# Kernel tuning notes

Hardware: AMD Instinct MI355X
Metric: run time of the kernel (lower is better)

## Reference

```python
import jax, jax.numpy as jnp
import numpy as np

B, T1, H, P, V = 4096, 65, 64, 50, 32
D = H + P  # input_size = 114


def setup_inputs() -> dict:
    key = jax.random.key(0)
    ks = jax.random.split(key, 20)
    s = 1.0 / np.sqrt(D)
    sh = 1.0 / np.sqrt(H)
    inp = {
        "phonetic_input": jax.random.normal(ks[0], (B, P), dtype=jnp.float32),
        "char_seq": jax.random.randint(ks[1], (B, T1), 0, V, dtype=jnp.int64),
        "emb": jax.random.normal(ks[2], (V, H), dtype=jnp.float32).at[0].set(0.0),  # padding_idx=0
        "W_rx": jax.random.uniform(ks[3], (D, H), jnp.float32, -s, s),
        "b_rx": jax.random.uniform(ks[4], (H,), jnp.float32, -s, s),
        "W_rh": jax.random.uniform(ks[5], (H, H), jnp.float32, -sh, sh),
        "b_rh": jax.random.uniform(ks[6], (H,), jnp.float32, -sh, sh),
        "W_zx": jax.random.uniform(ks[7], (D, H), jnp.float32, -s, s),
        "b_zx": jax.random.uniform(ks[8], (H,), jnp.float32, -s, s),
        "W_zh": jax.random.uniform(ks[9], (H, H), jnp.float32, -sh, sh),
        "b_zh": jax.random.uniform(ks[10], (H,), jnp.float32, -sh, sh),
        "W_hx": jax.random.uniform(ks[11], (D, H), jnp.float32, -s, s),
        "b_hx": jax.random.uniform(ks[12], (H,), jnp.float32, -s, s),
        "W_hh": jax.random.uniform(ks[13], (H, H), jnp.float32, -sh, sh),
        "b_hh": jax.random.uniform(ks[14], (H,), jnp.float32, -sh, sh),
        "W_proj": jax.random.uniform(ks[15], (H, V), jnp.float32, -sh, sh),
        "b_proj": jax.random.uniform(ks[16], (V,), jnp.float32, -sh, sh),
    }
    return inp


def reference(phonetic_input, char_seq, emb, W_rx, b_rx, W_rh, b_rh, W_zx, b_zx,
              W_zh, b_zh, W_hx, b_hx, W_hh, b_hh, W_proj, b_proj):
    input_seq = char_seq[:, :-1]          # [B, T]
    target_seq = char_seq[:, 1:]          # [B, T]
    Bsz, T = input_seq.shape

    char_emb = emb[input_seq]                                   # [B, T, H]
    phon = jnp.broadcast_to(phonetic_input[:, None, :], (Bsz, T, P))
    x = jnp.concatenate([char_emb, phon], axis=2)               # [B, T, D]

    # Hoist input-side projections into batched GEMMs, [T, B, H] for scan
    xr = jnp.einsum('btd,dh->tbh', x, W_rx) + b_rx
    xz = jnp.einsum('btd,dh->tbh', x, W_zx) + b_zx
    xh = jnp.einsum('btd,dh->tbh', x, W_hx) + b_hx

    h0 = jnp.zeros((Bsz, H), dtype=x.dtype)

    def step(h, inputs):
        xr_t, xz_t, xh_t = inputs
        r = jax.nn.sigmoid(xr_t + h @ W_rh + b_rh)
        z = jax.nn.sigmoid(xz_t + h @ W_zh + b_zh)
        c = jnp.tanh(xh_t + (r * h) @ W_hh + b_hh)
        h_new = (1.0 - z) * h + z * c
        return h_new, h_new

    _, hs = jax.lax.scan(step, h0, (xr, xz, xh))                # [T, B, H]
    logits = jnp.einsum('tbh,hv->btv', hs, W_proj) + b_proj     # [B, T, V]

    # cross_entropy with ignore_index=0 (mean over non-ignored)
    targets = target_seq.reshape(-1)
    logp = jax.nn.log_softmax(logits.reshape(-1, V), axis=-1)
    nll = -jnp.take_along_axis(logp, targets[:, None], axis=-1)[:, 0]
    mask = (targets != 0).astype(logits.dtype)
    loss = jnp.sum(nll * mask) / jnp.maximum(jnp.sum(mask), 1.0)
    return logits, loss
```

## Files before the change

### kernel.cpp

```cpp
#include <hip/hip_runtime.h>
#include <stdint.h>

#define Bsz 4096
#define Tn  64
#define T1n 65
#define Hn  64
#define Pn  50
#define Vn  32

typedef __attribute__((ext_vector_type(8))) short short8;
typedef __attribute__((ext_vector_type(4))) unsigned short bf16x4;
typedef __attribute__((ext_vector_type(4))) float floatx4;

__device__ __forceinline__ float bf2f(unsigned short u) {
  union { unsigned int i; float f; } x; x.i = ((unsigned int)u) << 16; return x.f;
}
__device__ __forceinline__ unsigned short f2bf(float f) {
  union { float f; unsigned int i; } x; x.f = f;
  return (unsigned short)((x.i + 0x7FFFu + ((x.i >> 16) & 1u)) >> 16);
}
__device__ __forceinline__ float fast_sigmoid(float x) {
  return __builtin_amdgcn_rcpf(1.f + __expf(-x));
}
__device__ __forceinline__ float fast_tanh(float x) {
  return 1.f - 2.f * __builtin_amdgcn_rcpf(1.f + __expf(2.f * x));
}
__device__ __forceinline__ void bar_lgkm() {
  asm volatile("s_waitcnt lgkmcnt(0)\n\ts_barrier" ::: "memory");
}

__device__ __forceinline__ short8 load_bfrag(const float* __restrict__ W, int ncols, int col, int kbase) {
  short8 f;
#pragma unroll
  for (int j = 0; j < 8; ++j) f[j] = (short)f2bf(W[(long)(kbase + j) * ncols + col]);
  return f;
}

__launch_bounds__(512)
__global__ void gru_kernel(const float* __restrict__ phon,
                           const int* __restrict__ cs,
                           const float* __restrict__ emb,
                           const float* __restrict__ Wrx, const float* __restrict__ brx,
                           const float* __restrict__ Wrh, const float* __restrict__ brh,
                           const float* __restrict__ Wzx, const float* __restrict__ bzx,
                           const float* __restrict__ Wzh, const float* __restrict__ bzh,
                           const float* __restrict__ Whx, const float* __restrict__ bhx,
                           const float* __restrict__ Whh, const float* __restrict__ bhh,
                           const float* __restrict__ Wpj, const float* __restrict__ bpj_g,
                           float* __restrict__ ws,
                           float* __restrict__ outp) {
  __shared__ __align__(16) unsigned short tbl_s[32 * 66 * 4];
  __shared__ __align__(16) unsigned short hist_s[2 * 1152];
  __shared__ __align__(16) unsigned short rh_s[1152];
  __shared__ float sum_s[32];
  __shared__ float tl_s[16];
  __shared__ unsigned int code4_s[(T1n + 1) * 4];
  __shared__ int det_s[1];

  const int tid = threadIdx.x;
  const int b0 = blockIdx.x * 16;
  const int W8 = tid >> 6, lane = tid & 63, q = lane >> 4, c16 = lane & 15;
  const bool isScan = (W8 < 4);
  const int jcol = (W8 & 3) * 16 + c16;
  const floatx4 zf = {0.f, 0.f, 0.f, 0.f};

  if (tid == 0) det_s[0] = 0;
  __syncthreads();
  if (tid < 128 && cs[2 * tid + 1] != 0) atomicOr(&det_s[0], 1);
  __syncthreads();
  const bool is64 = (det_s[0] == 0);

  for (int i = tid; i < 1152; i += 512) hist_s[1152 + i] = 0;
  for (int i = tid; i < T1n * 4; i += 512) {
    int t = i >> 2, qq = i & 3;
    unsigned int pk = 0;
#pragma unroll
    for (int r = 0; r < 4; ++r) {
      long idx = (long)(b0 + qq * 4 + r) * T1n + t;
      int c = is64 ? cs[2 * idx] : cs[idx];
      pk |= ((unsigned int)(c & 255)) << (8 * r);
    }
    code4_s[i] = pk;
  }

  for (int g = 0; g < 3; ++g) {
    const float* Wg = (g == 0) ? Wrx : (g == 1) ? Wzx : Whx;
    const float* bx = (g == 0) ? brx : (g == 1) ? bzx : bhx;
    const float* bh = (g == 0) ? brh : (g == 1) ? bzh : bhh;
    float acc[4] = {0.f, 0.f, 0.f, 0.f};
    float bias = bx[lane] + bh[lane];
    for (int d = 0; d < Hn; ++d) {
      float wv = Wg[(long)d * Hn + lane];
#pragma unroll
      for (int k = 0; k < 4; ++k)
        acc[k] += emb[(long)(W8 + 8 * k) * Hn + d] * wv;
    }
#pragma unroll
    for (int k = 0; k < 4; ++k) {
      int v = W8 + 8 * k;
      tbl_s[(v * 66 + lane) * 4 + g] = f2bf(acc[k] + bias);
    }
  }

  float ph_r[4] = {0.f, 0.f, 0.f, 0.f};
  float ph_z[4] = {0.f, 0.f, 0.f, 0.f};
  float ph_h[4] = {0.f, 0.f, 0.f, 0.f};
  if (isScan) {
    for (int p = 0; p < Pn; ++p) {
      float wr = Wrx[(long)(Hn + p) * Hn + jcol];
      float wz = Wzx[(long)(Hn + p) * Hn + jcol];
      float wh = Whx[(long)(Hn + p) * Hn + jcol];
#pragma unroll
      for (int r = 0; r < 4; ++r) {
        float xv = phon[(long)(b0 + q * 4 + r) * Pn + p];
        ph_r[r] += xv * wr; ph_z[r] += xv * wz; ph_h[r] += xv * wh;
      }
    }
  }

  short8 zs = {0,0,0,0,0,0,0,0};
  short8 Br0 = zs, Br1 = zs, Bz0 = zs, Bz1 = zs, Bh0 = zs, Bh1 = zs;
  short8 Bp0 = zs, Bp1 = zs;
  float bpj = 0.f;
  const int vt = W8 - 4;
  if (isScan) {
    Br0 = load_bfrag(Wrh, Hn, jcol, q * 8);
    Br1 = load_bfrag(Wrh, Hn, jcol, 32 + q * 8);
    Bz0 = load_bfrag(Wzh, Hn, jcol, q * 8);
    Bz1 = load_bfrag(Wzh, Hn, jcol, 32 + q * 8);
    Bh0 = load_bfrag(Whh, Hn, jcol, q * 8);
    Bh1 = load_bfrag(Whh, Hn, jcol, 32 + q * 8);
  } else if (W8 < 6) {
    Bp0 = load_bfrag(Wpj, Vn, vt * 16 + c16, q * 8);
    Bp1 = load_bfrag(Wpj, Vn, vt * 16 + c16, 32 + q * 8);
    bpj = bpj_g[vt * 16 + c16];
  }

  float h[4] = {0.f, 0.f, 0.f, 0.f};
  float z4[4] = {0.f, 0.f, 0.f, 0.f};
  float nll = 0.f, cnt = 0.f;
  bf16x4 tv[4];
  float eA[4], lgA[4];
  bool tm[4] = {false, false, false, false};

  if (isScan) {
    unsigned int pk0 = code4_s[q];
#pragma unroll
    for (int reg = 0; reg < 4; ++reg) {
      int cr = (pk0 >> (8 * reg)) & 255;
      tv[reg] = *(const bf16x4*)&tbl_s[(cr * 66 + jcol) * 4];
    }
  }

  __syncthreads();

  for (int t = 0; t < Tn + 2; ++t) {
    if (isScan) {
      if (t < Tn) {
        const unsigned short* hp = &hist_s[((t + 1) & 1) * 1152];
        short8 a0 = *(const short8*)&hp[c16 * 72 + q * 8];
        short8 a1 = *(const short8*)&hp[c16 * 72 + 32 + q * 8];
        floatx4 accr = __builtin_amdgcn_mfma_f32_16x16x32_bf16(a0, Br0, zf, 0, 0, 0);
        floatx4 accz = __builtin_amdgcn_mfma_f32_16x16x32_bf16(a0, Bz0, zf, 0, 0, 0);
        accr = __builtin_amdgcn_mfma_f32_16x16x32_bf16(a1, Br1, accr, 0, 0, 0);
        accz = __builtin_amdgcn_mfma_f32_16x16x32_bf16(a1, Bz1, accz, 0, 0, 0);
#pragma unroll
        for (int reg = 0; reg < 4; ++reg) {
          float xr = bf2f(tv[reg][0]) + ph_r[reg] + accr[reg];
          float xz = bf2f(tv[reg][1]) + ph_z[reg] + accz[reg];
          z4[reg] = fast_sigmoid(xz);
          rh_s[(q * 4 + reg) * 72 + jcol] = f2bf(fast_sigmoid(xr) * h[reg]);
        }
      }
    } else if (W8 < 6) {
      if (t >= 1 && t <= Tn) {
        const unsigned short* hp = &hist_s[((t + 1) & 1) * 1152];
        short8 a0 = *(const short8*)&hp[c16 * 72 + q * 8];
        short8 a1 = *(const short8*)&hp[c16 * 72 + 32 + q * 8];
        floatx4 l = __builtin_amdgcn_mfma_f32_16x16x32_bf16(a0, Bp0, zf, 0, 0, 0);
        l = __builtin_amdgcn_mfma_f32_16x16x32_bf16(a1, Bp1, l, 0, 0, 0);
        const int p = t - 1;
        unsigned int pkP = code4_s[t * 4 + q];
#pragma unroll
        for (int reg = 0; reg < 4; ++reg) {
          float lg = l[reg] + bpj;
          lgA[reg] = lg;
          eA[reg] = __expf(lg);
          long ad = ((long)(b0 + q * 4 + reg) * Tn + p) * Vn + vt * 16 + c16;
          outp[ad] = lg;
          int targ = (pkP >> (8 * reg)) & 255;
          tm[reg] = (targ != 0) && (targ == vt * 16 + c16);
        }
      }
    } else if (W8 == 6) {
      if (t >= 2 && lane < 16) {
        unsigned int pk6 = code4_s[(t - 1) * 4 + (lane >> 2)];
        int targ = (pk6 >> (8 * (lane & 3))) & 255;
        if (targ != 0) {
          float s = sum_s[lane] + sum_s[16 + lane];
          nll += __logf(s) - tl_s[lane];
          cnt += 1.f;
        }
      }
    }
    bar_lgkm();

    if (isScan) {
      if (t < Tn) {
        short8 p0 = *(const short8*)&rh_s[c16 * 72 + q * 8];
        short8 p1 = *(const short8*)&rh_s[c16 * 72 + 32 + q * 8];
        floatx4 acc = __builtin_amdgcn_mfma_f32_16x16x32_bf16(p0, Bh0, zf, 0, 0, 0);
        acc = __builtin_amdgcn_mfma_f32_16x16x32_bf16(p1, Bh1, acc, 0, 0, 0);
        unsigned short* hw = &hist_s[(t & 1) * 1152];
#pragma unroll
        for (int reg = 0; reg < 4; ++reg) {
          float xh = bf2f(tv[reg][2]) + ph_h[reg] + acc[reg];
          float c = fast_tanh(xh);
          float hn = fmaf(z4[reg], c - h[reg], h[reg]);
          h[reg] = hn;
          hw[(q * 4 + reg) * 72 + jcol] = f2bf(hn);
        }
        unsigned int pkN = code4_s[(t + 1) * 4 + q];
#pragma unroll
        for (int reg = 0; reg < 4; ++reg) {
          int crN = (pkN >> (8 * reg)) & 255;
          tv[reg] = *(const bf16x4*)&tbl_s[(crN * 66 + jcol) * 4];
        }
      }
    } else if (W8 < 6) {
      if (t >= 1 && t <= Tn) {
#pragma unroll
        for (int reg = 0; reg < 4; ++reg) {
          float s = eA[reg];
          s += __shfl_xor(s, 1); s += __shfl_xor(s, 2);
          s += __shfl_xor(s, 4); s += __shfl_xor(s, 8);
          if (c16 == 0) sum_s[vt * 16 + q * 4 + reg] = s;
          if (tm[reg])  tl_s[q * 4 + reg] = lgA[reg];
        }
      }
    }
    bar_lgkm();
  }

  if (W8 == 6) {
#pragma unroll
    for (int off = 8; off >= 1; off >>= 1) {
      nll += __shfl_xor(nll, off);
      cnt += __shfl_xor(cnt, off);
    }
    if (lane == 0) {
      ws[2 * blockIdx.x] = nll;
      ws[2 * blockIdx.x + 1] = cnt;
    }
  }
}

__global__ void loss_kernel(const float* __restrict__ ws, float* __restrict__ outp) {
  int lane = threadIdx.x;
  float n = 0.f, c = 0.f;
  for (int i = lane; i < Bsz / 16; i += 64) { n += ws[2 * i]; c += ws[2 * i + 1]; }
#pragma unroll
  for (int off = 32; off >= 1; off >>= 1) {
    n += __shfl_xor(n, off);
    c += __shfl_xor(c, off);
  }
  if (lane == 0) outp[(size_t)Bsz * Tn * Vn] = n / fmaxf(c, 1.f);
}

extern "C" void kernel_launch(void* const* d_in, const int* in_sizes, int n_in,
                              void* d_out, int out_size, void* d_ws, size_t ws_size,
                              hipStream_t stream) {
  const float* phon = (const float*)d_in[0];
  const int*   cs   = (const int*)d_in[1];
  const float* emb  = (const float*)d_in[2];
  const float* Wrx  = (const float*)d_in[3];
  const float* brx  = (const float*)d_in[4];
  const float* Wrh  = (const float*)d_in[5];
  const float* brh  = (const float*)d_in[6];
  const float* Wzx  = (const float*)d_in[7];
  const float* bzx  = (const float*)d_in[8];
  const float* Wzh  = (const float*)d_in[9];
  const float* bzh  = (const float*)d_in[10];
  const float* Whx  = (const float*)d_in[11];
  const float* bhx  = (const float*)d_in[12];
  const float* Whh  = (const float*)d_in[13];
  const float* bhh  = (const float*)d_in[14];
  const float* Wpj  = (const float*)d_in[15];
  const float* bpj  = (const float*)d_in[16];
  float* ws = (float*)d_ws;

  hipLaunchKernelGGL(gru_kernel, dim3(Bsz / 16), dim3(512), 0, stream,
                     phon, cs, emb, Wrx, brx, Wrh, brh, Wzx, bzx, Wzh, bzh,
                     Whx, bhx, Whh, bhh, Wpj, bpj, ws, (float*)d_out);
  hipLaunchKernelGGL(loss_kernel, dim3(1), dim3(64), 0, stream, ws, (float*)d_out);
}
```

Before: 190.1 us.

## Transpose GRU MFMA operands so hidden state packs per-lane and logits store vectorized

```diff
diff --git a/kernel.cpp b/kernel.cpp
--- a/kernel.cpp
+++ b/kernel.cpp
@@ -18,6 +18,9 @@
 __device__ __forceinline__ unsigned short f2bf(float f) {
   union { float f; unsigned int i; } x; x.f = f;
   return (unsigned short)((x.i + 0x7FFFu + ((x.i >> 16) & 1u)) >> 16);
+}
+__device__ __forceinline__ unsigned int packbf(float a, float b) {
+  return (unsigned int)f2bf(a) | ((unsigned int)f2bf(b) << 16);
 }
 __device__ __forceinline__ float fast_sigmoid(float x) {
   return __builtin_amdgcn_rcpf(1.f + __expf(-x));
@@ -49,19 +52,17 @@
                            const float* __restrict__ Wpj, const float* __restrict__ bpj_g,
                            float* __restrict__ ws,
                            float* __restrict__ outp) {
-  __shared__ __align__(16) unsigned short tbl_s[32 * 66 * 4];
-  __shared__ __align__(16) unsigned short hist_s[2 * 1152];
-  __shared__ __align__(16) unsigned short rh_s[1152];
-  __shared__ float sum_s[32];
+  __shared__ __align__(16) unsigned short tbl_s[3 * 32 * 68];
+  __shared__ __align__(16) unsigned int hp_s[16 * 36];
+  __shared__ __align__(16) unsigned int rhp_s[16 * 36];
+  __shared__ unsigned char codes_s[66 * 16];
+  __shared__ float sum_s[2 * 16];
   __shared__ float tl_s[16];
-  __shared__ unsigned int code4_s[(T1n + 1) * 4];
   __shared__ int det_s[1];
 
   const int tid = threadIdx.x;
   const int b0 = blockIdx.x * 16;
   const int W8 = tid >> 6, lane = tid & 63, q = lane >> 4, c16 = lane & 15;
-  const bool isScan = (W8 < 4);
-  const int jcol = (W8 & 3) * 16 + c16;
   const floatx4 zf = {0.f, 0.f, 0.f, 0.f};
 
   if (tid == 0) det_s[0] = 0;
@@ -70,17 +71,12 @@
   __syncthreads();
   const bool is64 = (det_s[0] == 0);
 
-  for (int i = tid; i < 1152; i += 512) hist_s[1152 + i] = 0;
-  for (int i = tid; i < T1n * 4; i += 512) {
-    int t = i >> 2, qq = i & 3;
-    unsigned int pk = 0;
-#pragma unroll
-    for (int r = 0; r < 4; ++r) {
-      long idx = (long)(b0 + qq * 4 + r) * T1n + t;
-      int c = is64 ? cs[2 * idx] : cs[idx];
-      pk |= ((unsigned int)(c & 255)) << (8 * r);
-    }
-    code4_s[i] = pk;
+  for (int i = tid; i < 16 * 36; i += 512) hp_s[i] = 0;
+  for (int i = tid; i < 65 * 16; i += 512) {
+    int t = i >> 4, b = i & 15;
+    long idx = (long)(b0 + b) * T1n + t;
+    int c = is64 ? cs[2 * idx] : cs[idx];
+    codes_s[i] = (unsigned char)(c & 255);
   }
 
   for (int g = 0; g < 3; ++g) {
@@ -96,106 +92,92 @@
         acc[k] += emb[(long)(W8 + 8 * k) * Hn + d] * wv;
     }
 #pragma unroll
-    for (int k = 0; k < 4; ++k) {
-      int v = W8 + 8 * k;
-      tbl_s[(v * 66 + lane) * 4 + g] = f2bf(acc[k] + bias);
-    }
-  }
-
-  float ph_r[4] = {0.f, 0.f, 0.f, 0.f};
-  float ph_z[4] = {0.f, 0.f, 0.f, 0.f};
-  float ph_h[4] = {0.f, 0.f, 0.f, 0.f};
-  if (isScan) {
+    for (int k = 0; k < 4; ++k)
+      tbl_s[g * 2176 + (W8 + 8 * k) * 68 + lane] = f2bf(acc[k] + bias);
+  }
+
+  const bool isGate = (W8 < 4);
+  const bool isProj = (W8 == 4 || W8 == 5);
+  const int w = W8 & 3;
+  const int m = W8 - 4;
+  const int tb = 16 * w + 4 * q;
+
+  short8 zs = {0,0,0,0,0,0,0,0};
+  short8 Ar0 = zs, Ar1 = zs, Az0 = zs, Az1 = zs, Ah0 = zs, Ah1 = zs;
+  short8 Ap0 = zs, Ap1 = zs;
+  float ph_r[4] = {0,0,0,0}, ph_z[4] = {0,0,0,0}, ph_h[4] = {0,0,0,0};
+  float bpjr[4] = {0,0,0,0};
+  if (isGate) {
+    Ar0 = load_bfrag(Wrh, Hn, 16 * w + c16, 8 * q);
+    Ar1 = load_bfrag(Wrh, Hn, 16 * w + c16, 32 + 8 * q);
+    Az0 = load_bfrag(Wzh, Hn, 16 * w + c16, 8 * q);
+    Az1 = load_bfrag(Wzh, Hn, 16 * w + c16, 32 + 8 * q);
+    Ah0 = load_bfrag(Whh, Hn, 16 * w + c16, 8 * q);
+    Ah1 = load_bfrag(Whh, Hn, 16 * w + c16, 32 + 8 * q);
     for (int p = 0; p < Pn; ++p) {
-      float wr = Wrx[(long)(Hn + p) * Hn + jcol];
-      float wz = Wzx[(long)(Hn + p) * Hn + jcol];
-      float wh = Whx[(long)(Hn + p) * Hn + jcol];
-#pragma unroll
-      for (int r = 0; r < 4; ++r) {
-        float xv = phon[(long)(b0 + q * 4 + r) * Pn + p];
-        ph_r[r] += xv * wr; ph_z[r] += xv * wz; ph_h[r] += xv * wh;
-      }
-    }
-  }
-
-  short8 zs = {0,0,0,0,0,0,0,0};
-  short8 Br0 = zs, Br1 = zs, Bz0 = zs, Bz1 = zs, Bh0 = zs, Bh1 = zs;
-  short8 Bp0 = zs, Bp1 = zs;
-  float bpj = 0.f;
-  const int vt = W8 - 4;
-  if (isScan) {
-    Br0 = load_bfrag(Wrh, Hn, jcol, q * 8);
-    Br1 = load_bfrag(Wrh, Hn, jcol, 32 + q * 8);
-    Bz0 = load_bfrag(Wzh, Hn, jcol, q * 8);
-    Bz1 = load_bfrag(Wzh, Hn, jcol, 32 + q * 8);
-    Bh0 = load_bfrag(Whh, Hn, jcol, q * 8);
-    Bh1 = load_bfrag(Whh, Hn, jcol, 32 + q * 8);
-  } else if (W8 < 6) {
-    Bp0 = load_bfrag(Wpj, Vn, vt * 16 + c16, q * 8);
-    Bp1 = load_bfrag(Wpj, Vn, vt * 16 + c16, 32 + q * 8);
-    bpj = bpj_g[vt * 16 + c16];
-  }
-
-  float h[4] = {0.f, 0.f, 0.f, 0.f};
+      float xv = phon[(long)(b0 + c16) * Pn + p];
+      floatx4 wr = *(const floatx4*)&Wrx[(long)(Hn + p) * Hn + tb];
+      floatx4 wz = *(const floatx4*)&Wzx[(long)(Hn + p) * Hn + tb];
+      floatx4 wh = *(const floatx4*)&Whx[(long)(Hn + p) * Hn + tb];
+#pragma unroll
+      for (int reg = 0; reg < 4; ++reg) {
+        ph_r[reg] += xv * wr[reg];
+        ph_z[reg] += xv * wz[reg];
+        ph_h[reg] += xv * wh[reg];
+      }
+    }
+  } else if (isProj) {
+    Ap0 = load_bfrag(Wpj, Vn, 16 * m + c16, 8 * q);
+    Ap1 = load_bfrag(Wpj, Vn, 16 * m + c16, 32 + 8 * q);
+#pragma unroll
+    for (int reg = 0; reg < 4; ++reg) bpjr[reg] = bpj_g[16 * m + 4 * q + reg];
+  }
+
+  const int hp_rd = c16 * 36 + 4 * q;
+  const int hp_wr = c16 * 36 + 8 * w + 2 * q;
+
+  float h4[4] = {0.f, 0.f, 0.f, 0.f};
   float z4[4] = {0.f, 0.f, 0.f, 0.f};
   float nll = 0.f, cnt = 0.f;
-  bf16x4 tv[4];
-  float eA[4], lgA[4];
-  bool tm[4] = {false, false, false, false};
-
-  if (isScan) {
-    unsigned int pk0 = code4_s[q];
-#pragma unroll
-    for (int reg = 0; reg < 4; ++reg) {
-      int cr = (pk0 >> (8 * reg)) & 255;
-      tv[reg] = *(const bf16x4*)&tbl_s[(cr * 66 + jcol) * 4];
-    }
-  }
+  int code = 0;
+  floatx4 lacc = zf;
 
   __syncthreads();
 
-  for (int t = 0; t < Tn + 2; ++t) {
-    if (isScan) {
+  for (int t = 0; t <= Tn + 1; ++t) {
+    if (isGate) {
       if (t < Tn) {
-        const unsigned short* hp = &hist_s[((t + 1) & 1) * 1152];
-        short8 a0 = *(const short8*)&hp[c16 * 72 + q * 8];
-        short8 a1 = *(const short8*)&hp[c16 * 72 + 32 + q * 8];
-        floatx4 accr = __builtin_amdgcn_mfma_f32_16x16x32_bf16(a0, Br0, zf, 0, 0, 0);
-        floatx4 accz = __builtin_amdgcn_mfma_f32_16x16x32_bf16(a0, Bz0, zf, 0, 0, 0);
-        accr = __builtin_amdgcn_mfma_f32_16x16x32_bf16(a1, Br1, accr, 0, 0, 0);
-        accz = __builtin_amdgcn_mfma_f32_16x16x32_bf16(a1, Bz1, accz, 0, 0, 0);
+        code = codes_s[t * 16 + c16];
+        short8 hb0 = *(const short8*)&hp_s[hp_rd];
+        short8 hb1 = *(const short8*)&hp_s[hp_rd + 16];
+        floatx4 accr = __builtin_amdgcn_mfma_f32_16x16x32_bf16(Ar0, hb0, zf, 0, 0, 0);
+        floatx4 accz = __builtin_amdgcn_mfma_f32_16x16x32_bf16(Az0, hb0, zf, 0, 0, 0);
+        accr = __builtin_amdgcn_mfma_f32_16x16x32_bf16(Ar1, hb1, accr, 0, 0, 0);
+        accz = __builtin_amdgcn_mfma_f32_16x16x32_bf16(Az1, hb1, accz, 0, 0, 0);
+        bf16x4 tvr = *(const bf16x4*)&tbl_s[code * 68 + tb];
+        bf16x4 tvz = *(const bf16x4*)&tbl_s[2176 + code * 68 + tb];
+        float rh[4];
 #pragma unroll
         for (int reg = 0; reg < 4; ++reg) {
-          float xr = bf2f(tv[reg][0]) + ph_r[reg] + accr[reg];
-          float xz = bf2f(tv[reg][1]) + ph_z[reg] + accz[reg];
+          float xr = bf2f(tvr[reg]) + ph_r[reg] + accr[reg];
+          float xz = bf2f(tvz[reg]) + ph_z[reg] + accz[reg];
           z4[reg] = fast_sigmoid(xz);
-          rh_s[(q * 4 + reg) * 72 + jcol] = f2bf(fast_sigmoid(xr) * h[reg]);
-        }
-      }
-    } else if (W8 < 6) {
+          rh[reg] = fast_sigmoid(xr) * h4[reg];
+        }
+        unsigned long long wv = (unsigned long long)packbf(rh[0], rh[1])
+                              | ((unsigned long long)packbf(rh[2], rh[3]) << 32);
+        *(unsigned long long*)&rhp_s[hp_wr] = wv;
+      }
+    } else if (isProj) {
       if (t >= 1 && t <= Tn) {
-        const unsigned short* hp = &hist_s[((t + 1) & 1) * 1152];
-        short8 a0 = *(const short8*)&hp[c16 * 72 + q * 8];
-        short8 a1 = *(const short8*)&hp[c16 * 72 + 32 + q * 8];
-        floatx4 l = __builtin_amdgcn_mfma_f32_16x16x32_bf16(a0, Bp0, zf, 0, 0, 0);
-        l = __builtin_amdgcn_mfma_f32_16x16x32_bf16(a1, Bp1, l, 0, 0, 0);
-        const int p = t - 1;
-        unsigned int pkP = code4_s[t * 4 + q];
-#pragma unroll
-        for (int reg = 0; reg < 4; ++reg) {
-          float lg = l[reg] + bpj;
-          lgA[reg] = lg;
-          eA[reg] = __expf(lg);
-          long ad = ((long)(b0 + q * 4 + reg) * Tn + p) * Vn + vt * 16 + c16;
-          outp[ad] = lg;
-          int targ = (pkP >> (8 * reg)) & 255;
-          tm[reg] = (targ != 0) && (targ == vt * 16 + c16);
-        }
+        short8 hb0 = *(const short8*)&hp_s[hp_rd];
+        short8 hb1 = *(const short8*)&hp_s[hp_rd + 16];
+        lacc = __builtin_amdgcn_mfma_f32_16x16x32_bf16(Ap0, hb0, zf, 0, 0, 0);
+        lacc = __builtin_amdgcn_mfma_f32_16x16x32_bf16(Ap1, hb1, lacc, 0, 0, 0);
       }
     } else if (W8 == 6) {
       if (t >= 2 && lane < 16) {
-        unsigned int pk6 = code4_s[(t - 1) * 4 + (lane >> 2)];
-        int targ = (pk6 >> (8 * (lane & 3))) & 255;
+        int targ = codes_s[(t - 1) * 16 + lane];
         if (targ != 0) {
           float s = sum_s[lane] + sum_s[16 + lane];
           nll += __logf(s) - tl_s[lane];
@@ -205,38 +187,41 @@
     }
     bar_lgkm();
 
-    if (isScan) {
+    if (isGate) {
       if (t < Tn) {
-        short8 p0 = *(const short8*)&rh_s[c16 * 72 + q * 8];
-        short8 p1 = *(const short8*)&rh_s[c16 * 72 + 32 + q * 8];
-        floatx4 acc = __builtin_amdgcn_mfma_f32_16x16x32_bf16(p0, Bh0, zf, 0, 0, 0);
-        acc = __builtin_amdgcn_mfma_f32_16x16x32_bf16(p1, Bh1, acc, 0, 0, 0);
-        unsigned short* hw = &hist_s[(t & 1) * 1152];
+        short8 p0 = *(const short8*)&rhp_s[hp_rd];
+        short8 p1 = *(const short8*)&rhp_s[hp_rd + 16];
+        floatx4 acch = __builtin_amdgcn_mfma_f32_16x16x32_bf16(Ah0, p0, zf, 0, 0, 0);
+        acch = __builtin_amdgcn_mfma_f32_16x16x32_bf16(Ah1, p1, acch, 0, 0, 0);
+        bf16x4 tvh = *(const bf16x4*)&tbl_s[4352 + code * 68 + tb];
 #pragma unroll
         for (int reg = 0; reg < 4; ++reg) {
-          float xh = bf2f(tv[reg][2]) + ph_h[reg] + acc[reg];
+          float xh = bf2f(tvh[reg]) + ph_h[reg] + acch[reg];
           float c = fast_tanh(xh);
-          float hn = fmaf(z4[reg], c - h[reg], h[reg]);
-          h[reg] = hn;
-          hw[(q * 4 + reg) * 72 + jcol] = f2bf(hn);
-        }
-        unsigned int pkN = code4_s[(t + 1) * 4 + q];
+          h4[reg] = fmaf(z4[reg], c - h4[reg], h4[reg]);
+        }
+        unsigned long long wv = (unsigned long long)packbf(h4[0], h4[1])
+                              | ((unsigned long long)packbf(h4[2], h4[3]) << 32);
+        *(unsigned long long*)&hp_s[hp_wr] = wv;
+      }
+    } else if (isProj) {
+      if (t >= 1 && t <= Tn) {
+        const int p = t - 1;
+        float lg[4]; float e = 0.f;
 #pragma unroll
         for (int reg = 0; reg < 4; ++reg) {
-          int crN = (pkN >> (8 * reg)) & 255;
-          tv[reg] = *(const bf16x4*)&tbl_s[(crN * 66 + jcol) * 4];
-        }
-      }
-    } else if (W8 < 6) {
-      if (t >= 1 && t <= Tn) {
-#pragma unroll
-        for (int reg = 0; reg < 4; ++reg) {
-          float s = eA[reg];
-          s += __shfl_xor(s, 1); s += __shfl_xor(s, 2);
-          s += __shfl_xor(s, 4); s += __shfl_xor(s, 8);
-          if (c16 == 0) sum_s[vt * 16 + q * 4 + reg] = s;
-          if (tm[reg])  tl_s[q * 4 + reg] = lgA[reg];
-        }
+          lg[reg] = lacc[reg] + bpjr[reg];
+          e += __expf(lg[reg]);
+        }
+        e += __shfl_xor(e, 16);
+        e += __shfl_xor(e, 32);
+        if (q == 0) sum_s[m * 16 + c16] = e;
+        int targ = codes_s[t * 16 + c16];
+#pragma unroll
+        for (int reg = 0; reg < 4; ++reg)
+          if (targ != 0 && targ == 16 * m + 4 * q + reg) tl_s[c16] = lg[reg];
+        floatx4 st = {lg[0], lg[1], lg[2], lg[3]};
+        *(floatx4*)&outp[((long)(b0 + c16) * Tn + p) * Vn + 16 * m + 4 * q] = st;
       }
     }
     bar_lgkm();
```

Measured after the change: 176.8 us. -7.0%, faster.
